# Kernel optimization log

Measured on AMD Instinct MI355X. Metric: run time of the kernel, lower is better.

## Reference

```python
import jax, jax.numpy as jnp
import numpy as np

N_HEADS = 8
DIM = 128
BT, A, M = 2880, 10, 350  # bs*T, agents, map tokens (from forwards())
TOPK_SELF, TOPK_CROSS = 3, 32


def _split_heads(x, h):
    B, T, C = x.shape
    return x.reshape(B, T, h, C // h).transpose(0, 2, 1, 3)  # [B,h,T,hd]


def _biased_attn(q, k, v, pe, rel):
    """flex_attention with score_mod: score + pe[b,q,rel[b,q,kv],h], -inf where rel==-1.
    q:[B,H,Tq,d] k,v:[B,H,Tk,d] pe:[B,Tq,K,H] rel:[B,Tq,Tk] int"""
    d = q.shape[-1]
    scores = jnp.einsum('bhqd,bhkd->bhqk', q, k) / jnp.sqrt(jnp.asarray(d, q.dtype))
    safe = jnp.maximum(rel, 0)
    bias = jnp.take_along_axis(pe, safe[:, :, :, None], axis=2)  # [B,Tq,Tk,H]
    bias = bias.transpose(0, 3, 1, 2)                            # [B,H,Tq,Tk]
    scores = jnp.where(rel[:, None, :, :] > -1, scores + bias, -jnp.inf)
    attn = jax.nn.softmax(scores, axis=-1)
    out = jnp.einsum('bhqk,bhkd->bhqd', attn, v)
    B, H, Tq, hd = out.shape
    return out.transpose(0, 2, 1, 3).reshape(B, Tq, H * hd)


def _make_relation(key, B, Tq, Tk, topk):
    # topk random keys per query get offsets 0..topk-1 in ascending kv order; rest -1
    rand = jax.random.uniform(key, (B, Tq, Tk))
    idx = jnp.sort(jax.lax.top_k(rand, topk)[1], axis=-1)  # [B,Tq,topk]
    rel = jnp.full((B, Tq, Tk), -1, dtype=jnp.int32)
    b = jnp.arange(B)[:, None, None]
    qi = jnp.arange(Tq)[None, :, None]
    return rel.at[b, qi, idx].set(jnp.arange(topk, dtype=jnp.int32)[None, None, :])


def setup_inputs() -> dict:
    key = jax.random.key(0)
    ks = jax.random.split(key, 12)
    s = 0.02
    return {
        'a_token': jax.random.normal(ks[0], (BT, A, DIM), jnp.float32),
        'm_token': jax.random.normal(ks[1], (BT, M, DIM), jnp.float32),
        'a2m_pe': jax.random.uniform(ks[2], (BT, A, TOPK_CROSS, N_HEADS), jnp.float32),
        'a_pe': jax.random.uniform(ks[3], (BT, A, TOPK_SELF, N_HEADS), jnp.float32),
        'Wq': s * jax.random.normal(ks[4], (DIM, DIM), jnp.float32),
        'Wk': s * jax.random.normal(ks[5], (DIM, DIM), jnp.float32),
        'Wv': s * jax.random.normal(ks[6], (DIM, DIM), jnp.float32),
        'W_cross_proj': s * jax.random.normal(ks[7], (DIM, DIM), jnp.float32),
        'W_cattn': s * jax.random.normal(ks[8], (DIM, 3 * DIM), jnp.float32),
        'W_self_proj': s * jax.random.normal(ks[9], (DIM, DIM), jnp.float32),
        'a2m_relation': _make_relation(ks[10], BT, A, M, TOPK_CROSS),
        'a_relation': _make_relation(ks[11], BT, A, A, TOPK_SELF),
    }


def reference(a_token, m_token, a2m_pe, a_pe, Wq, Wk, Wv, W_cross_proj,
              W_cattn, W_self_proj, a2m_relation, a_relation):
    # cross attention: q from a_token, k/v from m_token (dropout=0 => identity)
    q = _split_heads(a_token @ Wq, N_HEADS)
    k = _split_heads(m_token @ Wk, N_HEADS)
    v = _split_heads(m_token @ Wv, N_HEADS)
    y = _biased_attn(q, k, v, a2m_pe, a2m_relation) @ W_cross_proj
    # self attention with fused qkv projection
    q2, k2, v2 = jnp.split(y @ W_cattn, 3, axis=-1)
    y2 = _biased_attn(_split_heads(q2, N_HEADS), _split_heads(k2, N_HEADS),
                      _split_heads(v2, N_HEADS), a_pe, a_relation)
    return y2 @ W_self_proj
```

## Files before the change

### kernel.cpp

```cpp
#include <hip/hip_runtime.h>
#include <hip/hip_bf16.h>


typedef __attribute__((ext_vector_type(4))) float f32x4;
typedef __attribute__((ext_vector_type(8))) short bf16x8v;
typedef __attribute__((ext_vector_type(4))) short short4v;

#define BT_N 2880
#define A_N  10
#define M_N  350
#define BQ_N (BT_N * A_N)
#define DIMC 128

static __device__ __forceinline__ short f2b(float x) {
    __hip_bfloat16 b = __float2bfloat16(x);
    return __builtin_bit_cast(short, b);
}
static __device__ __forceinline__ float b2f(short s) {
    unsigned u = ((unsigned)(unsigned short)s) << 16;
    return __builtin_bit_cast(float, u);
}

__global__ __launch_bounds__(256) void precompute_mats(
    const float* __restrict__ Wq, const float* __restrict__ Wk,
    const float* __restrict__ Wv, const float* __restrict__ Wcp,
    const float* __restrict__ Wc, const float* __restrict__ Wsp,
    short* __restrict__ S1t, short* __restrict__ VP1t,
    short* __restrict__ S2t, short* __restrict__ VP2t)
{
    int gid = blockIdx.x * 256 + threadIdx.x;
    int mat = gid >> 17;
    int idx = gid & 131071;
    float acc = 0.f;
    if (mat == 0) {
        int n = idx >> 7, c = idx & 127;
        int h = n >> 7, d = n & 127;
        #pragma unroll
        for (int t = 0; t < 16; ++t)
            acc += Wq[c * 128 + h * 16 + t] * Wk[d * 128 + h * 16 + t];
        S1t[idx] = f2b(acc * 0.25f);
    } else if (mat == 1) {
        int d = idx >> 10, o = idx & 1023;
        int h = o >> 7, c = o & 127;
        #pragma unroll
        for (int t = 0; t < 16; ++t)
            acc += Wv[c * 128 + h * 16 + t] * Wcp[(h * 16 + t) * 128 + d];
        VP1t[idx] = f2b(acc);
    } else if (mat == 2) {
        int n = idx >> 7, c = idx & 127;
        int h = n >> 7, d = n & 127;
        #pragma unroll
        for (int t = 0; t < 16; ++t)
            acc += Wc[c * 384 + h * 16 + t] * Wc[d * 384 + 128 + h * 16 + t];
        S2t[idx] = f2b(acc * 0.25f);
    } else {
        int d = idx >> 10, o = idx & 1023;
        int h = o >> 7, c = o & 127;
        #pragma unroll
        for (int t = 0; t < 16; ++t)
            acc += Wc[c * 384 + 256 + h * 16 + t] * Wsp[(h * 16 + t) * 128 + d];
        VP2t[idx] = f2b(acc);
    }
}

__global__ __launch_bounds__(256) void conv_bf16(
    const float* __restrict__ in, short* __restrict__ out)
{
    int i = blockIdx.x * 256 + threadIdx.x;
    f32x4 a = ((const f32x4*)in)[2 * i];
    f32x4 b = ((const f32x4*)in)[2 * i + 1];
    bf16x8v t;
    t[0] = f2b(a.x); t[1] = f2b(a.y); t[2] = f2b(a.z); t[3] = f2b(a.w);
    t[4] = f2b(b.x); t[5] = f2b(b.y); t[6] = f2b(b.z); t[7] = f2b(b.w);
    ((bf16x8v*)out)[i] = t;
}

template<bool CF32>
__global__ __launch_bounds__(256) void gemm_bt(
    const short* __restrict__ Ap, const short* __restrict__ Bt,
    void* __restrict__ Cp, int M, int N, int K)
{
    __shared__ short As[128][72];
    __shared__ short Bs[128][72];
    const int tid  = threadIdx.x;
    const int bm   = blockIdx.y << 7, bn = blockIdx.x << 7;
    const int wave = tid >> 6, lane = tid & 63;
    const int wm   = (wave >> 1) << 6, wn = (wave & 1) << 6;
    const int row16 = lane & 15, kq = (lane >> 4) << 3;
    f32x4 acc[4][4] = {};

    for (int k0 = 0; k0 < K; k0 += 64) {
        #pragma unroll
        for (int i = 0; i < 4; ++i) {
            int g = (i << 8) + tid;
            int r = g >> 3, c = (g & 7) << 3;
            *(bf16x8v*)&As[r][c] = *(const bf16x8v*)(Ap + (size_t)(bm + r) * K + k0 + c);
        }
        #pragma unroll
        for (int i = 0; i < 4; ++i) {
            int g = (i << 8) + tid;
            int r = g >> 3, c = (g & 7) << 3;
            *(bf16x8v*)&Bs[r][c] = *(const bf16x8v*)(Bt + (size_t)(bn + r) * K + k0 + c);
        }
        __syncthreads();
        #pragma unroll
        for (int kk = 0; kk < 64; kk += 32) {
            bf16x8v afr[4], bfr[4];
            #pragma unroll
            for (int mi = 0; mi < 4; ++mi)
                afr[mi] = *(const bf16x8v*)&As[wm + (mi << 4) + row16][kq + kk];
            #pragma unroll
            for (int ni = 0; ni < 4; ++ni)
                bfr[ni] = *(const bf16x8v*)&Bs[wn + (ni << 4) + row16][kq + kk];
            #pragma unroll
            for (int mi = 0; mi < 4; ++mi)
                #pragma unroll
                for (int ni = 0; ni < 4; ++ni)
                    acc[mi][ni] = __builtin_amdgcn_mfma_f32_16x16x32_bf16(
                        afr[mi], bfr[ni], acc[mi][ni], 0, 0, 0);
        }
        __syncthreads();
    }

    const int col = lane & 15, rb = (lane >> 4) << 2;
    #pragma unroll
    for (int mi = 0; mi < 4; ++mi)
        #pragma unroll
        for (int ni = 0; ni < 4; ++ni)
            #pragma unroll
            for (int r = 0; r < 4; ++r) {
                int rr = bm + wm + (mi << 4) + rb + r;
                int cc = bn + wn + (ni << 4) + col;
                float v = acc[mi][ni][r];
                if (CF32) ((float*)Cp)[(size_t)rr * N + cc] = v;
                else      ((short*)Cp)[(size_t)rr * N + cc] = f2b(v);
            }
}

__global__ __launch_bounds__(256) void attn_cross(
    const float* __restrict__ m_token, const short* __restrict__ qS,
    const float* __restrict__ pe, const int* __restrict__ rel,
    short* __restrict__ u)
{
    __shared__ float mrows[32][132];
    __shared__ float qsr[1024];
    __shared__ int   selk[32];
    __shared__ float wts[8][32];
    const int phys = blockIdx.x;
    const int b    = (phys & 7) * 360 + (phys >> 3) / A_N;
    const int q    = (phys >> 3) % A_N;
    const int bq   = b * A_N + q;
    const int tid = threadIdx.x;

    const int* relrow = rel + (size_t)bq * M_N;
    for (int k = tid; k < M_N; k += 256) {
        int r = relrow[k];
        if (r >= 0) selk[r] = k;
    }
    {
        short4v v = ((const short4v*)(qS + (size_t)bq * 1024))[tid];
        qsr[(tid << 2) + 0] = b2f(v.x);
        qsr[(tid << 2) + 1] = b2f(v.y);
        qsr[(tid << 2) + 2] = b2f(v.z);
        qsr[(tid << 2) + 3] = b2f(v.w);
    }
    __syncthreads();
    #pragma unroll
    for (int i = 0; i < 4; ++i) {
        int f = (i << 8) + tid;
        int r = f >> 5, c = (f & 31) << 2;
        f32x4 v = *(const f32x4*)(m_token + ((size_t)b * M_N + selk[r]) * DIMC + c);
        *(f32x4*)&mrows[r][c] = v;
    }
    __syncthreads();
    {
        const int h = tid >> 5, r = tid & 31;
        const float* qh = qsr + (h << 7);
        f32x4 p = {0.f, 0.f, 0.f, 0.f};
        #pragma unroll
        for (int d = 0; d < DIMC; d += 4)
            p += *(const f32x4*)(qh + d) * *(const f32x4*)&mrows[r][d];
        float sc = p.x + p.y + p.z + p.w + pe[((size_t)bq * 32 + r) * 8 + h];
        float mx = sc;
        #pragma unroll
        for (int off = 16; off; off >>= 1) mx = fmaxf(mx, __shfl_xor(mx, off, 32));
        float e = __expf(sc - mx);
        float s = e;
        #pragma unroll
        for (int off = 16; off; off >>= 1) s += __shfl_xor(s, off, 32);
        wts[h][r] = e / s;
    }
    __syncthreads();
    {
        const int h = tid >> 5, d0 = (tid << 2) & 127;
        f32x4 acc = {0.f, 0.f, 0.f, 0.f};
        #pragma unroll
        for (int r = 0; r < 32; ++r)
            acc += wts[h][r] * *(const f32x4*)&mrows[r][d0];
        short4v t;
        t.x = f2b(acc.x); t.y = f2b(acc.y); t.z = f2b(acc.z); t.w = f2b(acc.w);
        *(short4v*)(u + (size_t)bq * 1024 + (tid << 2)) = t;
    }
}

__global__ __launch_bounds__(256) void attn_self(
    const short* __restrict__ ybf, const short* __restrict__ yS2,
    const float* __restrict__ pe, const int* __restrict__ rel,
    short* __restrict__ u2)
{
    __shared__ float yrows[3][132];
    __shared__ float ysr[1024];
    __shared__ int   selk[3];
    __shared__ float sw[8][3];
    const int bq = blockIdx.x;
    const int b  = bq / A_N;
    const int tid = threadIdx.x;

    if (tid < A_N) {
        int r = rel[(size_t)bq * A_N + tid];
        if (r >= 0) selk[r] = tid;
    }
    {
        short4v v = ((const short4v*)(yS2 + (size_t)bq * 1024))[tid];
        ysr[(tid << 2) + 0] = b2f(v.x);
        ysr[(tid << 2) + 1] = b2f(v.y);
        ysr[(tid << 2) + 2] = b2f(v.z);
        ysr[(tid << 2) + 3] = b2f(v.w);
    }
    __syncthreads();
    if (tid < 48) {
        int r = tid >> 4, c = (tid & 15) << 3;
        bf16x8v v = *(const bf16x8v*)(ybf + ((size_t)b * A_N + selk[r]) * DIMC + c);
        #pragma unroll
        for (int j = 0; j < 8; ++j) yrows[r][c + j] = b2f(v[j]);
    }
    __syncthreads();
    if (tid < 24) {
        int h = tid / 3, r = tid - h * 3;
        const float* qh = ysr + (h << 7);
        f32x4 p = {0.f, 0.f, 0.f, 0.f};
        #pragma unroll
        for (int d = 0; d < DIMC; d += 4)
            p += *(const f32x4*)(qh + d) * *(const f32x4*)&yrows[r][d];
        sw[h][r] = p.x + p.y + p.z + p.w + pe[((size_t)bq * 3 + r) * 8 + h];
    }
    __syncthreads();
    if (tid < 8) {
        float s0 = sw[tid][0], s1 = sw[tid][1], s2 = sw[tid][2];
        float mx = fmaxf(s0, fmaxf(s1, s2));
        float e0 = __expf(s0 - mx), e1 = __expf(s1 - mx), e2 = __expf(s2 - mx);
        float inv = 1.f / (e0 + e1 + e2);
        sw[tid][0] = e0 * inv; sw[tid][1] = e1 * inv; sw[tid][2] = e2 * inv;
    }
    __syncthreads();
    {
        const int h = tid >> 5, d0 = (tid << 2) & 127;
        f32x4 acc = sw[h][0] * *(const f32x4*)&yrows[0][d0]
                  + sw[h][1] * *(const f32x4*)&yrows[1][d0]
                  + sw[h][2] * *(const f32x4*)&yrows[2][d0];
        short4v t;
        t.x = f2b(acc.x); t.y = f2b(acc.y); t.z = f2b(acc.z); t.w = f2b(acc.w);
        *(short4v*)(u2 + (size_t)bq * 1024 + (tid << 2)) = t;
    }
}

extern "C" void kernel_launch(void* const* d_in, const int* in_sizes, int n_in,
                              void* d_out, int out_size, void* d_ws, size_t ws_size,
                              hipStream_t stream)
{
    const float* a_token = (const float*)d_in[0];
    const float* m_token = (const float*)d_in[1];
    const float* a2m_pe  = (const float*)d_in[2];
    const float* a_pe    = (const float*)d_in[3];
    const float* Wq      = (const float*)d_in[4];
    const float* Wk      = (const float*)d_in[5];
    const float* Wv      = (const float*)d_in[6];
    const float* Wcp     = (const float*)d_in[7];
    const float* Wc      = (const float*)d_in[8];
    const float* Wsp     = (const float*)d_in[9];
    const int*   a2m_rel = (const int*)d_in[10];
    const int*   a_rel   = (const int*)d_in[11];

    char* ws = (char*)d_ws;
    short* S1t  = (short*)(ws + 0);
    short* VP1t = (short*)(ws + 262144);
    short* S2t  = (short*)(ws + 524288);
    short* VP2t = (short*)(ws + 786432);
    short* buf1 = (short*)(ws + 1048576);
    short* buf2 = (short*)(ws + 1048576 + 58982400ull);
    short* ybf  = (short*)(ws + 1048576 + 2ull * 58982400ull);
    short* abf  = (short*)(ws + 1048576 + 2ull * 58982400ull + 7372800ull);
    float* outp = (float*)d_out;

    precompute_mats<<<dim3(2048), dim3(256), 0, stream>>>(
        Wq, Wk, Wv, Wcp, Wc, Wsp, S1t, VP1t, S2t, VP2t);

    conv_bf16<<<dim3(1800), dim3(256), 0, stream>>>(a_token, abf);

    gemm_bt<false><<<dim3(8, 225), dim3(256), 0, stream>>>(
        abf, S1t, (void*)buf1, BQ_N, 1024, 128);

    attn_cross<<<dim3(BQ_N), dim3(256), 0, stream>>>(
        m_token, buf1, a2m_pe, a2m_rel, buf2);

    gemm_bt<false><<<dim3(1, 225), dim3(256), 0, stream>>>(
        buf2, VP1t, (void*)ybf, BQ_N, 128, 1024);

    gemm_bt<false><<<dim3(8, 225), dim3(256), 0, stream>>>(
        ybf, S2t, (void*)buf1, BQ_N, 1024, 128);

    attn_self<<<dim3(BQ_N), dim3(256), 0, stream>>>(
        ybf, buf1, a_pe, a_rel, buf2);

    gemm_bt<true><<<dim3(1, 225), dim3(256), 0, stream>>>(
        buf2, VP2t, (void*)outp, BQ_N, 128, 1024);
}
```

Before: 294.8 us.

## Batch self-attention per sequence and use 64-row GEMM tiles for N=128 projections

Adds a 64x128-tile GEMM variant for the two K=1024, N=128 projection GEMMs, doubling the block count from 225 to 450 so more of the GPU's compute units stay busy. The self-attention kernel is restructured so one block handles all 10 queries of a batch element instead of one query per block. It loads the 10 key rows, the relation entries and the bias once and spreads the dot products over 240 threads rather than 24. This reduces redundant loads and idle threads, but uses more shared memory per block (about 46 KB), which may limit occupancy.

```diff
diff --git a/kernel.cpp b/kernel.cpp
--- a/kernel.cpp
+++ b/kernel.cpp
@@ -125,6 +125,68 @@
     const int col = lane & 15, rb = (lane >> 4) << 2;
     #pragma unroll
     for (int mi = 0; mi < 4; ++mi)
+        #pragma unroll
+        for (int ni = 0; ni < 4; ++ni)
+            #pragma unroll
+            for (int r = 0; r < 4; ++r) {
+                int rr = bm + wm + (mi << 4) + rb + r;
+                int cc = bn + wn + (ni << 4) + col;
+                float v = acc[mi][ni][r];
+                if (CF32) ((float*)Cp)[(size_t)rr * N + cc] = v;
+                else      ((short*)Cp)[(size_t)rr * N + cc] = f2b(v);
+            }
+}
+
+template<bool CF32>
+__global__ __launch_bounds__(256) void gemm_bt64(
+    const short* __restrict__ Ap, const short* __restrict__ Bt,
+    void* __restrict__ Cp, int M, int N, int K)
+{
+    __shared__ short As[64][72];
+    __shared__ short Bs[128][72];
+    const int tid  = threadIdx.x;
+    const int bm   = blockIdx.y << 6, bn = blockIdx.x << 7;
+    const int wave = tid >> 6, lane = tid & 63;
+    const int wm   = (wave >> 1) << 5, wn = (wave & 1) << 6;
+    const int row16 = lane & 15, kq = (lane >> 4) << 3;
+    f32x4 acc[2][4] = {};
+
+    for (int k0 = 0; k0 < K; k0 += 64) {
+        #pragma unroll
+        for (int i = 0; i < 2; ++i) {
+            int g = (i << 8) + tid;
+            int r = g >> 3, c = (g & 7) << 3;
+            *(bf16x8v*)&As[r][c] = *(const bf16x8v*)(Ap + (size_t)(bm + r) * K + k0 + c);
+        }
+        #pragma unroll
+        for (int i = 0; i < 4; ++i) {
+            int g = (i << 8) + tid;
+            int r = g >> 3, c = (g & 7) << 3;
+            *(bf16x8v*)&Bs[r][c] = *(const bf16x8v*)(Bt + (size_t)(bn + r) * K + k0 + c);
+        }
+        __syncthreads();
+        #pragma unroll
+        for (int kk = 0; kk < 64; kk += 32) {
+            bf16x8v afr[2], bfr[4];
+            #pragma unroll
+            for (int mi = 0; mi < 2; ++mi)
+                afr[mi] = *(const bf16x8v*)&As[wm + (mi << 4) + row16][kq + kk];
+            #pragma unroll
+            for (int ni = 0; ni < 4; ++ni)
+                bfr[ni] = *(const bf16x8v*)&Bs[wn + (ni << 4) + row16][kq + kk];
+            #pragma unroll
+            for (int mi = 0; mi < 2; ++mi)
+                #pragma unroll
+                for (int ni = 0; ni < 4; ++ni)
+                    acc[mi][ni] = __builtin_amdgcn_mfma_f32_16x16x32_bf16(
+                        afr[mi], bfr[ni], acc[mi][ni], 0, 0, 0);
+        }
+        __syncthreads();
+    }
+
+    const int col = lane & 15, rb = (lane >> 4) << 2;
+    #pragma unroll
+    for (int mi = 0; mi < 2; ++mi)
         #pragma unroll
         for (int ni = 0; ni < 4; ++ni)
             #pragma unroll
@@ -203,64 +265,80 @@
     }
 }
 
-__global__ __launch_bounds__(256) void attn_self(
+__global__ __launch_bounds__(256) void attn_self_b(
     const short* __restrict__ ybf, const short* __restrict__ yS2,
     const float* __restrict__ pe, const int* __restrict__ rel,
     short* __restrict__ u2)
 {
-    __shared__ float yrows[3][132];
-    __shared__ float ysr[1024];
-    __shared__ int   selk[3];
-    __shared__ float sw[8][3];
-    const int bq = blockIdx.x;
-    const int b  = bq / A_N;
+    __shared__ float ysr[10][1024];
+    __shared__ float yrows[10][132];
+    __shared__ float sw[10][8][3];
+    __shared__ float peL[240];
+    __shared__ int   selk[30];
+    const int b   = blockIdx.x;
     const int tid = threadIdx.x;
 
-    if (tid < A_N) {
-        int r = rel[(size_t)bq * A_N + tid];
-        if (r >= 0) selk[r] = tid;
-    }
-    {
-        short4v v = ((const short4v*)(yS2 + (size_t)bq * 1024))[tid];
-        ysr[(tid << 2) + 0] = b2f(v.x);
-        ysr[(tid << 2) + 1] = b2f(v.y);
-        ysr[(tid << 2) + 2] = b2f(v.z);
-        ysr[(tid << 2) + 3] = b2f(v.w);
-    }
-    __syncthreads();
-    if (tid < 48) {
-        int r = tid >> 4, c = (tid & 15) << 3;
-        bf16x8v v = *(const bf16x8v*)(ybf + ((size_t)b * A_N + selk[r]) * DIMC + c);
-        #pragma unroll
-        for (int j = 0; j < 8; ++j) yrows[r][c + j] = b2f(v[j]);
-    }
-    __syncthreads();
-    if (tid < 24) {
-        int h = tid / 3, r = tid - h * 3;
-        const float* qh = ysr + (h << 7);
+    #pragma unroll
+    for (int i = 0; i < 5; ++i) {
+        int g = (i << 8) + tid;
+        int r = g >> 7, c8 = (g & 127) << 3;
+        bf16x8v v = *(const bf16x8v*)(yS2 + ((size_t)b * A_N + r) * 1024 + c8);
+        f32x4 lo = {b2f(v[0]), b2f(v[1]), b2f(v[2]), b2f(v[3])};
+        f32x4 hi = {b2f(v[4]), b2f(v[5]), b2f(v[6]), b2f(v[7])};
+        *(f32x4*)&ysr[r][c8] = lo;
+        *(f32x4*)&ysr[r][c8 + 4] = hi;
+    }
+    if (tid < 160) {
+        int r = tid >> 4, c8 = (tid & 15) << 3;
+        bf16x8v v = *(const bf16x8v*)(ybf + ((size_t)b * A_N + r) * DIMC + c8);
+        #pragma unroll
+        for (int j = 0; j < 8; ++j) yrows[r][c8 + j] = b2f(v[j]);
+    }
+    if (tid < 100) {
+        int v = rel[(size_t)b * 100 + tid];
+        if (v >= 0) selk[(tid / 10) * 3 + v] = tid % 10;
+    }
+    if (tid < 240) peL[tid] = pe[(size_t)b * 240 + tid];
+    __syncthreads();
+
+    if (tid < 240) {
+        int q = tid / 24, rem = tid - q * 24;
+        int h = rem >> 2, r = rem & 3;
+        h = rem / 3; r = rem - h * 3;
+        int k = selk[q * 3 + r];
+        const float* qh = &ysr[q][h << 7];
+        const float* yk = &yrows[k][0];
         f32x4 p = {0.f, 0.f, 0.f, 0.f};
         #pragma unroll
         for (int d = 0; d < DIMC; d += 4)
-            p += *(const f32x4*)(qh + d) * *(const f32x4*)&yrows[r][d];
-        sw[h][r] = p.x + p.y + p.z + p.w + pe[((size_t)bq * 3 + r) * 8 + h];
-    }
-    __syncthreads();
-    if (tid < 8) {
-        float s0 = sw[tid][0], s1 = sw[tid][1], s2 = sw[tid][2];
+            p += *(const f32x4*)(qh + d) * *(const f32x4*)(yk + d);
+        sw[q][h][r] = p.x + p.y + p.z + p.w + peL[q * 24 + r * 8 + h];
+    }
+    __syncthreads();
+
+    if (tid < 80) {
+        int q = tid >> 3, h = tid & 7;
+        float s0 = sw[q][h][0], s1 = sw[q][h][1], s2 = sw[q][h][2];
         float mx = fmaxf(s0, fmaxf(s1, s2));
         float e0 = __expf(s0 - mx), e1 = __expf(s1 - mx), e2 = __expf(s2 - mx);
         float inv = 1.f / (e0 + e1 + e2);
-        sw[tid][0] = e0 * inv; sw[tid][1] = e1 * inv; sw[tid][2] = e2 * inv;
-    }
-    __syncthreads();
-    {
-        const int h = tid >> 5, d0 = (tid << 2) & 127;
-        f32x4 acc = sw[h][0] * *(const f32x4*)&yrows[0][d0]
-                  + sw[h][1] * *(const f32x4*)&yrows[1][d0]
-                  + sw[h][2] * *(const f32x4*)&yrows[2][d0];
+        sw[q][h][0] = e0 * inv; sw[q][h][1] = e1 * inv; sw[q][h][2] = e2 * inv;
+    }
+    __syncthreads();
+
+    #pragma unroll
+    for (int i = 0; i < 10; ++i) {
+        int g = (i << 8) + tid;
+        int q = g >> 8, rem = g & 255;
+        int h = rem >> 5, c4 = (rem & 31) << 2;
+        int k0 = selk[q * 3 + 0], k1 = selk[q * 3 + 1], k2 = selk[q * 3 + 2];
+        float w0 = sw[q][h][0], w1 = sw[q][h][1], w2 = sw[q][h][2];
+        f32x4 acc = w0 * *(const f32x4*)&yrows[k0][c4]
+                  + w1 * *(const f32x4*)&yrows[k1][c4]
+                  + w2 * *(const f32x4*)&yrows[k2][c4];
         short4v t;
         t.x = f2b(acc.x); t.y = f2b(acc.y); t.z = f2b(acc.z); t.w = f2b(acc.w);
-        *(short4v*)(u2 + (size_t)bq * 1024 + (tid << 2)) = t;
+        *(short4v*)(u2 + ((size_t)b * A_N + q) * 1024 + (h << 7) + c4) = t;
     }
 }
 
@@ -303,15 +381,15 @@
     attn_cross<<<dim3(BQ_N), dim3(256), 0, stream>>>(
         m_token, buf1, a2m_pe, a2m_rel, buf2);
 
-    gemm_bt<false><<<dim3(1, 225), dim3(256), 0, stream>>>(
+    gemm_bt64<false><<<dim3(1, 450), dim3(256), 0, stream>>>(
         buf2, VP1t, (void*)ybf, BQ_N, 128, 1024);
 
     gemm_bt<false><<<dim3(8, 225), dim3(256), 0, stream>>>(
         ybf, S2t, (void*)buf1, BQ_N, 1024, 128);
 
-    attn_self<<<dim3(BQ_N), dim3(256), 0, stream>>>(
+    attn_self_b<<<dim3(BT_N), dim3(256), 0, stream>>>(
         ybf, buf1, a_pe, a_rel, buf2);
 
-    gemm_bt<true><<<dim3(1, 225), dim3(256), 0, stream>>>(
+    gemm_bt64<true><<<dim3(1, 450), dim3(256), 0, stream>>>(
         buf2, VP2t, (void*)outp, BQ_N, 128, 1024);
 }
```

After: 330.8 us. 1.12x slower.

## Use bf16 MFMA for cross-attention scores with bf16 shared tiles

Applied to the files above, without the earlier changes.

The cross-attention kernel now stores the gathered map rows and per-head queries in shared memory as bf16 and computes the 32x8 score matrix with 16x16x32 bf16 MFMA instructions on two waves, replacing the per-thread fp32 dot products. The positional bias is staged in shared memory with one coalesced load, and the weighted-value sum reads the bf16 rows. This cuts shared memory use and scalar FMA work but rounds the map tokens to bf16, which loses precision, and it leaves two waves idle during the score step.

```diff
diff --git a/kernel.cpp b/kernel.cpp
--- a/kernel.cpp
+++ b/kernel.cpp
@@ -142,61 +142,92 @@
     const float* __restrict__ pe, const int* __restrict__ rel,
     short* __restrict__ u)
 {
-    __shared__ float mrows[32][132];
-    __shared__ float qsr[1024];
+    __shared__ short mrows[32][136];
+    __shared__ short qsr[16][136];
+    __shared__ float sc[32][17];
+    __shared__ float wts[8][33];
+    __shared__ float peL[256];
     __shared__ int   selk[32];
-    __shared__ float wts[8][32];
+
     const int phys = blockIdx.x;
     const int b    = (phys & 7) * 360 + (phys >> 3) / A_N;
     const int q    = (phys >> 3) % A_N;
     const int bq   = b * A_N + q;
-    const int tid = threadIdx.x;
+    const int tid  = threadIdx.x;
+    const int wave = tid >> 6, lane = tid & 63;
+    const int row16 = lane & 15, kq8 = (lane >> 4) << 3;
 
     const int* relrow = rel + (size_t)bq * M_N;
     for (int k = tid; k < M_N; k += 256) {
         int r = relrow[k];
         if (r >= 0) selk[r] = k;
     }
-    {
-        short4v v = ((const short4v*)(qS + (size_t)bq * 1024))[tid];
-        qsr[(tid << 2) + 0] = b2f(v.x);
-        qsr[(tid << 2) + 1] = b2f(v.y);
-        qsr[(tid << 2) + 2] = b2f(v.z);
-        qsr[(tid << 2) + 3] = b2f(v.w);
-    }
-    __syncthreads();
-    #pragma unroll
-    for (int i = 0; i < 4; ++i) {
-        int f = (i << 8) + tid;
-        int r = f >> 5, c = (f & 31) << 2;
-        f32x4 v = *(const f32x4*)(m_token + ((size_t)b * M_N + selk[r]) * DIMC + c);
-        *(f32x4*)&mrows[r][c] = v;
-    }
-    __syncthreads();
+    if (tid < 128) {
+        int h = tid >> 4, c8 = (tid & 15) << 3;
+        *(bf16x8v*)&qsr[h][c8] = *(const bf16x8v*)(qS + (size_t)bq * 1024 + h * 128 + c8);
+    }
+    for (int g = tid; g < 1088; g += 256) ((short*)qsr)[1088 + g] = 0;
+    peL[tid] = pe[(size_t)bq * 256 + tid];
+    __syncthreads();
+
+    {
+        int r = tid >> 3, c16 = (tid & 7) << 4;
+        const float* src = m_token + ((size_t)b * M_N + selk[r]) * DIMC + c16;
+        f32x4 v0 = *(const f32x4*)(src);
+        f32x4 v1 = *(const f32x4*)(src + 4);
+        f32x4 v2 = *(const f32x4*)(src + 8);
+        f32x4 v3 = *(const f32x4*)(src + 12);
+        bf16x8v t0, t1;
+        t0[0] = f2b(v0.x); t0[1] = f2b(v0.y); t0[2] = f2b(v0.z); t0[3] = f2b(v0.w);
+        t0[4] = f2b(v1.x); t0[5] = f2b(v1.y); t0[6] = f2b(v1.z); t0[7] = f2b(v1.w);
+        t1[0] = f2b(v2.x); t1[1] = f2b(v2.y); t1[2] = f2b(v2.z); t1[3] = f2b(v2.w);
+        t1[4] = f2b(v3.x); t1[5] = f2b(v3.y); t1[6] = f2b(v3.z); t1[7] = f2b(v3.w);
+        *(bf16x8v*)&mrows[r][c16]     = t0;
+        *(bf16x8v*)&mrows[r][c16 + 8] = t1;
+    }
+    __syncthreads();
+
+    if (wave < 2) {
+        f32x4 acc = {0.f, 0.f, 0.f, 0.f};
+        #pragma unroll
+        for (int kc = 0; kc < 4; ++kc) {
+            bf16x8v a  = *(const bf16x8v*)&mrows[(wave << 4) + row16][(kc << 5) + kq8];
+            bf16x8v bb = *(const bf16x8v*)&qsr[row16][(kc << 5) + kq8];
+            acc = __builtin_amdgcn_mfma_f32_16x16x32_bf16(a, bb, acc, 0, 0, 0);
+        }
+        const int rb4 = (lane >> 4) << 2;
+        #pragma unroll
+        for (int r = 0; r < 4; ++r)
+            sc[(wave << 4) + rb4 + r][row16] = acc[r];
+    }
+    __syncthreads();
+
     {
         const int h = tid >> 5, r = tid & 31;
-        const float* qh = qsr + (h << 7);
-        f32x4 p = {0.f, 0.f, 0.f, 0.f};
-        #pragma unroll
-        for (int d = 0; d < DIMC; d += 4)
-            p += *(const f32x4*)(qh + d) * *(const f32x4*)&mrows[r][d];
-        float sc = p.x + p.y + p.z + p.w + pe[((size_t)bq * 32 + r) * 8 + h];
-        float mx = sc;
+        float s = sc[r][h] + peL[r * 8 + h];
+        float mx = s;
         #pragma unroll
         for (int off = 16; off; off >>= 1) mx = fmaxf(mx, __shfl_xor(mx, off, 32));
-        float e = __expf(sc - mx);
-        float s = e;
-        #pragma unroll
-        for (int off = 16; off; off >>= 1) s += __shfl_xor(s, off, 32);
-        wts[h][r] = e / s;
-    }
-    __syncthreads();
+        float e = __expf(s - mx);
+        float su = e;
+        #pragma unroll
+        for (int off = 16; off; off >>= 1) su += __shfl_xor(su, off, 32);
+        wts[h][r] = e / su;
+    }
+    __syncthreads();
+
     {
         const int h = tid >> 5, d0 = (tid << 2) & 127;
         f32x4 acc = {0.f, 0.f, 0.f, 0.f};
         #pragma unroll
-        for (int r = 0; r < 32; ++r)
-            acc += wts[h][r] * *(const f32x4*)&mrows[r][d0];
+        for (int r = 0; r < 32; ++r) {
+            float w = wts[h][r];
+            short4v mv = *(const short4v*)&mrows[r][d0];
+            acc.x += w * b2f(mv.x);
+            acc.y += w * b2f(mv.y);
+            acc.z += w * b2f(mv.z);
+            acc.w += w * b2f(mv.w);
+        }
         short4v t;
         t.x = f2b(acc.x); t.y = f2b(acc.y); t.z = f2b(acc.z); t.w = f2b(acc.w);
         *(short4v*)(u + (size_t)bq * 1024 + (tid << 2)) = t;
```

Result: faster. 288.2 us (-2.2%).
